# Kernel tuning notes

Measured on AMD Instinct MI355X. Metric: run time of the kernel, lower is better.

The kernel has to match this reference:

```python
import jax, jax.numpy as jnp
import numpy as np

N_NODES = 100000
N_EDGES = 1600000
NEG_SLOPE = 0.01  # F.leaky_relu default


def _param(key, shape, scale=0.05):
    return jax.random.normal(key, shape, dtype=jnp.float32) * scale


def setup_inputs() -> dict:
    key = jax.random.key(0)
    ks = jax.random.split(key, 32)
    inp = {
        "x": jax.random.normal(ks[0], (N_NODES, 64), dtype=jnp.float32),
        "edge_index": jax.random.randint(ks[1], (2, N_EDGES), 0, N_NODES, dtype=jnp.int64),
        # encoder SAGEConv params: lin_l (neighbors, with bias) + lin_r (root)
        "ggn1_Wl": _param(ks[2], (128, 64)), "ggn1_b": jnp.zeros((128,), jnp.float32), "ggn1_Wr": _param(ks[3], (128, 64)),
        "ggn2_Wl": _param(ks[4], (128, 128)), "ggn2_b": jnp.zeros((128,), jnp.float32), "ggn2_Wr": _param(ks[5], (128, 128)),
        "ggn3_Wl": _param(ks[6], (128, 128)), "ggn3_b": jnp.zeros((128,), jnp.float32), "ggn3_Wr": _param(ks[7], (128, 128)),
        "tr2_W": _param(ks[8], (64, 128)), "tr2_b": jnp.zeros((64,), jnp.float32),
        # decoder
        "dec1_W": _param(ks[9], (128, 64)), "dec1_b": jnp.zeros((128,), jnp.float32),
        "dec2_Wl": _param(ks[10], (128, 128)), "dec2_b": jnp.zeros((128,), jnp.float32), "dec2_Wr": _param(ks[11], (128, 128)),
        "dec3_Wl": _param(ks[12], (64, 128)), "dec3_b": jnp.zeros((64,), jnp.float32), "dec3_Wr": _param(ks[13], (64, 128)),
        "dec4_Wl": _param(ks[14], (3, 64)), "dec4_b": jnp.zeros((3,), jnp.float32), "dec4_Wr": _param(ks[15], (3, 64)),
    }
    return inp


def _sage(x, src, dst, Wl, b, Wr, n):
    # PyG SAGEConv (aggr='mean'): lin_l(mean_{j->i} x_j) + lin_r(x_i)
    msgs = x[src]                                              # [E, d] gather
    s = jax.ops.segment_sum(msgs, dst, num_segments=n)          # [N, d]
    cnt = jax.ops.segment_sum(jnp.ones((src.shape[0], 1), x.dtype), dst, num_segments=n)
    mean = s / jnp.maximum(cnt, 1.0)
    return mean @ Wl.T + b + x @ Wr.T


def _leaky(h):
    return jnp.where(h > 0, h, NEG_SLOPE * h)


def reference(x, edge_index,
              ggn1_Wl, ggn1_b, ggn1_Wr,
              ggn2_Wl, ggn2_b, ggn2_Wr,
              ggn3_Wl, ggn3_b, ggn3_Wr,
              tr2_W, tr2_b,
              dec1_W, dec1_b,
              dec2_Wl, dec2_b, dec2_Wr,
              dec3_Wl, dec3_b, dec3_Wr,
              dec4_Wl, dec4_b, dec4_Wr):
    n = x.shape[0]
    src, dst = edge_index[0], edge_index[1]  # source_to_target flow
    # --- encode (dropout = identity, deterministic reference) ---
    h = jnp.tanh(_sage(x, src, dst, ggn1_Wl, ggn1_b, ggn1_Wr, n))
    h = jnp.tanh(_sage(h, src, dst, ggn2_Wl, ggn2_b, ggn2_Wr, n))
    h = jnp.tanh(_sage(h, src, dst, ggn3_Wl, ggn3_b, ggn3_Wr, n))
    mu = h @ tr2_W.T + tr2_b
    logvar = mu  # module applies the same tr2 twice
    z = mu       # reparametrize in eval mode returns mu
    # --- decode ---
    o = _leaky(z @ dec1_W.T + dec1_b)
    o = _leaky(_sage(o, src, dst, dec2_Wl, dec2_b, dec2_Wr, n))
    o = jnp.tanh(_sage(o, src, dst, dec3_Wl, dec3_b, dec3_Wr, n))
    z2 = _sage(o, src, dst, dec4_Wl, dec4_b, dec4_Wr, n)
    return (z2[:, :2], z2[:, 2], mu, logvar)
```

## Files before the change

kernel.cpp:

```cpp
#include <hip/hip_runtime.h>
#include <cmath>


constexpr int ACT_NONE = 0, ACT_TANH = 1, ACT_LEAKY = 2;
constexpr int SCAN_CHUNK = 4096;

typedef __attribute__((ext_vector_type(8))) __bf16 bf16x8;
typedef __attribute__((ext_vector_type(4))) float f32x4;

__device__ __forceinline__ unsigned short f2h(float x) {
  _Float16 h = (_Float16)x;
  unsigned short u;
  __builtin_memcpy(&u, &h, 2);
  return u;
}
__device__ __forceinline__ float hlo(unsigned int u) {
  unsigned short s = (unsigned short)(u & 0xffffu);
  _Float16 h;
  __builtin_memcpy(&h, &s, 2);
  return (float)h;
}
__device__ __forceinline__ float hhi(unsigned int u) {
  unsigned short s = (unsigned short)(u >> 16);
  _Float16 h;
  __builtin_memcpy(&h, &s, 2);
  return (float)h;
}

__global__ __launch_bounds__(256) void count_rank_kernel(const int* __restrict__ dst,
                                                         int* __restrict__ cnt,
                                                         int* __restrict__ rank, int E) {
  int e = blockIdx.x * 256 + threadIdx.x;
  if (e < E) rank[e] = atomicAdd(&cnt[dst[e]], 1);
}

__global__ __launch_bounds__(1024) void scan_blk_kernel(const int* __restrict__ cnt,
                                                        int* __restrict__ rowptr,
                                                        float* __restrict__ inv,
                                                        int* __restrict__ bsum, int n) {
  __shared__ int wsum[17];
  const int lane = threadIdx.x & 63;
  const int wid = threadIdx.x >> 6;
  const int i0 = blockIdx.x * SCAN_CHUNK + threadIdx.x * 4;
  int v[4];
  if (i0 + 3 < n) {
    int4 t = *(const int4*)(cnt + i0);
    v[0] = t.x; v[1] = t.y; v[2] = t.z; v[3] = t.w;
  } else {
#pragma unroll
    for (int j = 0; j < 4; ++j) v[j] = (i0 + j < n) ? cnt[i0 + j] : 0;
  }
#pragma unroll
  for (int j = 0; j < 4; ++j)
    if (i0 + j < n) inv[i0 + j] = 1.0f / (float)(v[j] > 1 ? v[j] : 1);
  const int s = v[0] + v[1] + v[2] + v[3];
  int x = s;
#pragma unroll
  for (int off = 1; off < 64; off <<= 1) {
    int t = __shfl_up(x, off);
    if (lane >= off) x += t;
  }
  if (lane == 63) wsum[wid + 1] = x;
  __syncthreads();
  if (threadIdx.x == 0) {
    wsum[0] = 0;
    for (int w = 1; w <= 16; ++w) wsum[w] += wsum[w - 1];
    bsum[blockIdx.x] = wsum[16];
  }
  __syncthreads();
  int p = wsum[wid] + x - s;
#pragma unroll
  for (int j = 0; j < 4; ++j) {
    if (i0 + j < n) rowptr[i0 + j] = p;
    p += v[j];
  }
}

__global__ __launch_bounds__(1024) void scan_sums_kernel(int* __restrict__ bsum,
                                                         int* __restrict__ rowptr,
                                                         int nb, int n) {
  __shared__ int wsum[17];
  const int lane = threadIdx.x & 63;
  const int wid = threadIdx.x >> 6;
  const int v = (threadIdx.x < nb) ? bsum[threadIdx.x] : 0;
  int x = v;
#pragma unroll
  for (int off = 1; off < 64; off <<= 1) {
    int t = __shfl_up(x, off);
    if (lane >= off) x += t;
  }
  if (lane == 63) wsum[wid + 1] = x;
  __syncthreads();
  if (threadIdx.x == 0) {
    wsum[0] = 0;
    for (int w = 1; w <= 16; ++w) wsum[w] += wsum[w - 1];
    rowptr[n] = wsum[16];
  }
  __syncthreads();
  if (threadIdx.x < nb) bsum[threadIdx.x] = wsum[wid] + x - v;
}

__global__ __launch_bounds__(1024) void scan_add_kernel(int* __restrict__ rowptr,
                                                        const int* __restrict__ bsum,
                                                        int n) {
  const int off = bsum[blockIdx.x];
  const int i0 = blockIdx.x * SCAN_CHUNK + threadIdx.x * 4;
  if (i0 + 3 < n) {
    int4 t = *(const int4*)(rowptr + i0);
    t.x += off; t.y += off; t.z += off; t.w += off;
    *(int4*)(rowptr + i0) = t;
  } else {
    for (int j = 0; j < 4; ++j)
      if (i0 + j < n) rowptr[i0 + j] += off;
  }
}

__global__ __launch_bounds__(256) void scatter_kernel(const int* __restrict__ src,
                                                      const int* __restrict__ dst,
                                                      const int* __restrict__ rowptr,
                                                      const int* __restrict__ rank,
                                                      int* __restrict__ esrc, int E) {
  int e = blockIdx.x * 256 + threadIdx.x;
  if (e < E) esrc[rowptr[dst[e]] + rank[e]] = src[e];
}

template <int D>
__global__ __launch_bounds__(256) void gather_mean_kernel(
    const float* __restrict__ in, const int* __restrict__ esrc,
    const int* __restrict__ rowptr, const float* __restrict__ inv,
    float* __restrict__ meanb, int n) {
  const int node = blockIdx.x * 4 + (threadIdx.x >> 6);
  const int lane = threadIdx.x & 63;
  if (node >= n) return;
  const int beg = rowptr[node];
  const int end = rowptr[node + 1];
  const float iv = inv[node];
  if constexpr (D == 128) {
    const float2* base = (const float2*)in;
    float a0x = 0.f, a0y = 0.f, a1x = 0.f, a1y = 0.f;
    float a2x = 0.f, a2y = 0.f, a3x = 0.f, a3y = 0.f;
    for (int b = beg; b < end; b += 64) {
      int m = end - b;
      if (m > 64) m = 64;
      int myi = (lane < m) ? esrc[b + lane] : 0;
      int s = 0;
      for (; s + 4 <= m; s += 4) {
        int i0 = __shfl(myi, s);
        int i1 = __shfl(myi, s + 1);
        int i2 = __shfl(myi, s + 2);
        int i3 = __shfl(myi, s + 3);
        float2 v0 = base[(size_t)i0 * 64 + lane];
        float2 v1 = base[(size_t)i1 * 64 + lane];
        float2 v2 = base[(size_t)i2 * 64 + lane];
        float2 v3 = base[(size_t)i3 * 64 + lane];
        a0x += v0.x; a0y += v0.y;
        a1x += v1.x; a1y += v1.y;
        a2x += v2.x; a2y += v2.y;
        a3x += v3.x; a3y += v3.y;
      }
      for (; s < m; ++s) {
        int i0 = __shfl(myi, s);
        float2 v0 = base[(size_t)i0 * 64 + lane];
        a0x += v0.x; a0y += v0.y;
      }
    }
    float2 r;
    r.x = ((a0x + a1x) + (a2x + a3x)) * iv;
    r.y = ((a0y + a1y) + (a2y + a3y)) * iv;
    ((float2*)meanb)[(size_t)node * 64 + lane] = r;
  } else {
    float a0 = 0.f, a1 = 0.f, a2 = 0.f, a3 = 0.f;
    for (int b = beg; b < end; b += 64) {
      int m = end - b;
      if (m > 64) m = 64;
      int myi = (lane < m) ? esrc[b + lane] : 0;
      int s = 0;
      for (; s + 4 <= m; s += 4) {
        int i0 = __shfl(myi, s);
        int i1 = __shfl(myi, s + 1);
        int i2 = __shfl(myi, s + 2);
        int i3 = __shfl(myi, s + 3);
        a0 += in[(size_t)i0 * 64 + lane];
        a1 += in[(size_t)i1 * 64 + lane];
        a2 += in[(size_t)i2 * 64 + lane];
        a3 += in[(size_t)i3 * 64 + lane];
      }
      for (; s < m; ++s) {
        int i0 = __shfl(myi, s);
        a0 += in[(size_t)i0 * 64 + lane];
      }
    }
    meanb[(size_t)node * 64 + lane] = ((a0 + a1) + (a2 + a3)) * iv;
  }
}

__global__ __launch_bounds__(256) void gather_s16_kernel(
    const unsigned short* __restrict__ inq, const int* __restrict__ esrc,
    const int* __restrict__ rowptr, const float* __restrict__ inv,
    float* __restrict__ meanb, int n) {
  const int node = blockIdx.x * 4 + (threadIdx.x >> 6);
  const int lane = threadIdx.x & 63;
  if (node >= n) return;
  const int beg = rowptr[node];
  const int end = rowptr[node + 1];
  const float iv = inv[node] * (1.0f / 32767.0f);
  const unsigned int* bu = (const unsigned int*)inq;
  int a0l = 0, a0h = 0, a1l = 0, a1h = 0;
  int a2l = 0, a2h = 0, a3l = 0, a3h = 0;
  for (int b = beg; b < end; b += 64) {
    int m = end - b;
    if (m > 64) m = 64;
    int myi = (lane < m) ? esrc[b + lane] : 0;
    int s = 0;
    for (; s + 4 <= m; s += 4) {
      int i0 = __shfl(myi, s);
      int i1 = __shfl(myi, s + 1);
      int i2 = __shfl(myi, s + 2);
      int i3 = __shfl(myi, s + 3);
      unsigned int u0 = bu[(size_t)i0 * 64 + lane];
      unsigned int u1 = bu[(size_t)i1 * 64 + lane];
      unsigned int u2 = bu[(size_t)i2 * 64 + lane];
      unsigned int u3 = bu[(size_t)i3 * 64 + lane];
      a0l += (int)(short)u0; a0h += ((int)u0) >> 16;
      a1l += (int)(short)u1; a1h += ((int)u1) >> 16;
      a2l += (int)(short)u2; a2h += ((int)u2) >> 16;
      a3l += (int)(short)u3; a3h += ((int)u3) >> 16;
    }
    for (; s < m; ++s) {
      int i0 = __shfl(myi, s);
      unsigned int u0 = bu[(size_t)i0 * 64 + lane];
      a0l += (int)(short)u0; a0h += ((int)u0) >> 16;
    }
  }
  float2 r;
  r.x = (float)((a0l + a1l) + (a2l + a3l)) * iv;
  r.y = (float)((a0h + a1h) + (a2h + a3h)) * iv;
  ((float2*)meanb)[(size_t)node * 64 + lane] = r;
}

template <int D>
__global__ __launch_bounds__(256) void gather_h_kernel(
    const unsigned short* __restrict__ inh, const int* __restrict__ esrc,
    const int* __restrict__ rowptr, const float* __restrict__ inv,
    float* __restrict__ meanb, int n) {
  const int node = blockIdx.x * 4 + (threadIdx.x >> 6);
  const int lane = threadIdx.x & 63;
  if (node >= n) return;
  const int beg = rowptr[node];
  const int end = rowptr[node + 1];
  const float iv = inv[node];
  const unsigned int* bu = (const unsigned int*)inh;
  if constexpr (D == 128) {
    float a0x = 0.f, a0y = 0.f, a1x = 0.f, a1y = 0.f;
    float a2x = 0.f, a2y = 0.f, a3x = 0.f, a3y = 0.f;
    for (int b = beg; b < end; b += 64) {
      int m = end - b;
      if (m > 64) m = 64;
      int myi = (lane < m) ? esrc[b + lane] : 0;
      int s = 0;
      for (; s + 4 <= m; s += 4) {
        int i0 = __shfl(myi, s);
        int i1 = __shfl(myi, s + 1);
        int i2 = __shfl(myi, s + 2);
        int i3 = __shfl(myi, s + 3);
        unsigned int u0 = bu[(size_t)i0 * 64 + lane];
        unsigned int u1 = bu[(size_t)i1 * 64 + lane];
        unsigned int u2 = bu[(size_t)i2 * 64 + lane];
        unsigned int u3 = bu[(size_t)i3 * 64 + lane];
        a0x += hlo(u0); a0y += hhi(u0);
        a1x += hlo(u1); a1y += hhi(u1);
        a2x += hlo(u2); a2y += hhi(u2);
        a3x += hlo(u3); a3y += hhi(u3);
      }
      for (; s < m; ++s) {
        int i0 = __shfl(myi, s);
        unsigned int u0 = bu[(size_t)i0 * 64 + lane];
        a0x += hlo(u0); a0y += hhi(u0);
      }
    }
    float2 r;
    r.x = ((a0x + a1x) + (a2x + a3x)) * iv;
    r.y = ((a0y + a1y) + (a2y + a3y)) * iv;
    ((float2*)meanb)[(size_t)node * 64 + lane] = r;
  } else {
    const int half = lane >> 5;
    const int hl = lane & 31;
    float ax = 0.f, ay = 0.f, bx = 0.f, by = 0.f;
    for (int b = beg; b < end; b += 64) {
      int m = end - b;
      if (m > 64) m = 64;
      int myi = (lane < m) ? esrc[b + lane] : 0;
      int s = 0;
      for (; s + 4 <= m; s += 4) {
        int i0 = __shfl(myi, s + half);
        int i1 = __shfl(myi, s + 2 + half);
        unsigned int u0 = bu[(size_t)i0 * 32 + hl];
        unsigned int u1 = bu[(size_t)i1 * 32 + hl];
        ax += hlo(u0); ay += hhi(u0);
        bx += hlo(u1); by += hhi(u1);
      }
      for (; s < m; s += 2) {
        int t = s + half;
        if (t < m) {
          int i0 = __shfl(myi, t);
          unsigned int u0 = bu[(size_t)i0 * 32 + hl];
          ax += hlo(u0); ay += hhi(u0);
        }
      }
    }
    float sx = ax + bx, sy = ay + by;
    sx += __shfl_xor(sx, 32);
    sy += __shfl_xor(sy, 32);
    if (half == 0)
      ((float2*)meanb)[(size_t)node * 32 + hl] = make_float2(sx * iv, sy * iv);
  }
}

__global__ __launch_bounds__(256) void gather_mean4_kernel(
    const float* __restrict__ y4, const int* __restrict__ esrc,
    const int* __restrict__ rowptr, const float* __restrict__ inv,
    float* __restrict__ mean4, int n) {
  int i = blockIdx.x * 256 + threadIdx.x;
  if (i >= n) return;
  const int beg = rowptr[i], end = rowptr[i + 1];
  const float iv = inv[i];
  float sx = 0.f, sy = 0.f, sz = 0.f;
  const float4* b = (const float4*)y4;
  for (int j = beg; j < end; ++j) {
    float4 v = b[esrc[j]];
    sx += v.x; sy += v.y; sz += v.z;
  }
  ((float4*)mean4)[i] = make_float4(sx * iv, sy * iv, sz * iv, 0.f);
}

__device__ __forceinline__ void split_bf16(float x, __bf16& h, __bf16& l) {
  h = (__bf16)x;
  l = (__bf16)(x - (float)h);
}

template <int DI, int DO, int ACT, bool AGG, bool ADDMEAN, bool BIAS, int SH>
__global__ __launch_bounds__(256) void node_mfma_kernel(
    const float* __restrict__ in, const float* __restrict__ meanb,
    const float* __restrict__ Wl, const float* __restrict__ Wr,
    const float* __restrict__ bias, float* __restrict__ out,
    float* __restrict__ out2, unsigned short* __restrict__ outh, int n) {
  constexpr int BM = 128;
  constexpr int KC = 32;
  constexpr int KS = 40;
  constexpr int CT = DO / 16;
  __shared__ __align__(16) __bf16 As_hi[BM * KS];
  __shared__ __align__(16) __bf16 As_lo[BM * KS];
  __shared__ __align__(16) __bf16 Ws_hi[DO * KS];
  __shared__ __align__(16) __bf16 Ws_lo[DO * KS];

  const int wv = threadIdx.x >> 6;
  const int lane = threadIdx.x & 63;
  const int lm = lane & 15;
  const int lq = lane >> 4;
  const int row0 = blockIdx.x * BM;

  f32x4 acc[2][CT];
#pragma unroll
  for (int rt = 0; rt < 2; ++rt)
#pragma unroll
    for (int ct = 0; ct < CT; ++ct) acc[rt][ct] = (f32x4){0.f, 0.f, 0.f, 0.f};

  const int nphase = AGG ? 2 : 1;
  for (int phase = 0; phase < nphase; ++phase) {
    const float* W = (phase == 0) ? Wr : Wl;
    const float* Amat = (phase == 0) ? in : meanb;
    for (int k0 = 0; k0 < DI; k0 += KC) {
      {
        const int r = threadIdx.x >> 1;
        const int kb = (threadIdx.x & 1) * 16;
        const int row = row0 + r;
        float v[16];
        if (row < n) {
          const float4* p = (const float4*)(Amat + (size_t)row * DI + k0 + kb);
#pragma unroll
          for (int i = 0; i < 4; ++i) {
            float4 t = p[i];
            v[4 * i + 0] = t.x; v[4 * i + 1] = t.y;
            v[4 * i + 2] = t.z; v[4 * i + 3] = t.w;
          }
        } else {
#pragma unroll
          for (int i = 0; i < 16; ++i) v[i] = 0.f;
        }
        bf16x8 hi[2], lo[2];
#pragma unroll
        for (int g = 0; g < 2; ++g)
#pragma unroll
          for (int i = 0; i < 8; ++i) {
            __bf16 h, l;
            split_bf16(v[g * 8 + i], h, l);
            hi[g][i] = h; lo[g][i] = l;
          }
        *(bf16x8*)(&As_hi[r * KS + kb]) = hi[0];
        *(bf16x8*)(&As_hi[r * KS + kb + 8]) = hi[1];
        *(bf16x8*)(&As_lo[r * KS + kb]) = lo[0];
        *(bf16x8*)(&As_lo[r * KS + kb + 8]) = lo[1];
      }
      if constexpr (DO == 128) {
        const int c = threadIdx.x >> 1;
        const int kb = (threadIdx.x & 1) * 16;
        const float4* p = (const float4*)(W + (size_t)c * DI + k0 + kb);
        float v[16];
#pragma unroll
        for (int i = 0; i < 4; ++i) {
          float4 t = p[i];
          v[4 * i + 0] = t.x; v[4 * i + 1] = t.y;
          v[4 * i + 2] = t.z; v[4 * i + 3] = t.w;
        }
        bf16x8 hi[2], lo[2];
#pragma unroll
        for (int g = 0; g < 2; ++g)
#pragma unroll
          for (int i = 0; i < 8; ++i) {
            __bf16 h, l;
            split_bf16(v[g * 8 + i], h, l);
            hi[g][i] = h; lo[g][i] = l;
          }
        *(bf16x8*)(&Ws_hi[c * KS + kb]) = hi[0];
        *(bf16x8*)(&Ws_hi[c * KS + kb + 8]) = hi[1];
        *(bf16x8*)(&Ws_lo[c * KS + kb]) = lo[0];
        *(bf16x8*)(&Ws_lo[c * KS + kb + 8]) = lo[1];
      } else {
        const int c = threadIdx.x >> 2;
        const int kb = (threadIdx.x & 3) * 8;
        const float4* p = (const float4*)(W + (size_t)c * DI + k0 + kb);
        float v[8];
#pragma unroll
        for (int i = 0; i < 2; ++i) {
          float4 t = p[i];
          v[4 * i + 0] = t.x; v[4 * i + 1] = t.y;
          v[4 * i + 2] = t.z; v[4 * i + 3] = t.w;
        }
        bf16x8 hi, lo;
#pragma unroll
        for (int i = 0; i < 8; ++i) {
          __bf16 h, l;
          split_bf16(v[i], h, l);
          hi[i] = h; lo[i] = l;
        }
        *(bf16x8*)(&Ws_hi[c * KS + kb]) = hi;
        *(bf16x8*)(&Ws_lo[c * KS + kb]) = lo;
      }
      __syncthreads();
      const int kb = lq * 8;
      bf16x8 ah[2], al[2];
#pragma unroll
      for (int rt = 0; rt < 2; ++rt) {
        const int r = wv * 32 + rt * 16 + lm;
        ah[rt] = *(const bf16x8*)(&As_hi[r * KS + kb]);
        al[rt] = *(const bf16x8*)(&As_lo[r * KS + kb]);
      }
#pragma unroll
      for (int ct = 0; ct < CT; ++ct) {
        const int c = ct * 16 + lm;
        bf16x8 bh = *(const bf16x8*)(&Ws_hi[c * KS + kb]);
        bf16x8 bl = *(const bf16x8*)(&Ws_lo[c * KS + kb]);
#pragma unroll
        for (int rt = 0; rt < 2; ++rt) {
          acc[rt][ct] = __builtin_amdgcn_mfma_f32_16x16x32_bf16(ah[rt], bh, acc[rt][ct], 0, 0, 0);
          acc[rt][ct] = __builtin_amdgcn_mfma_f32_16x16x32_bf16(al[rt], bh, acc[rt][ct], 0, 0, 0);
          acc[rt][ct] = __builtin_amdgcn_mfma_f32_16x16x32_bf16(ah[rt], bl, acc[rt][ct], 0, 0, 0);
        }
      }
      __syncthreads();
    }
  }

#pragma unroll
  for (int rt = 0; rt < 2; ++rt)
#pragma unroll
    for (int ct = 0; ct < CT; ++ct) {
      const int col = ct * 16 + lm;
      const float bval = BIAS ? bias[col] : 0.f;
      f32x4 a = acc[rt][ct];
#pragma unroll
      for (int r = 0; r < 4; ++r) {
        const int row = row0 + wv * 32 + rt * 16 + lq * 4 + r;
        if (row < n) {
          float t = a[r] + bval;
          if (ADDMEAN) t += meanb[(size_t)row * DO + col];
          if (ACT == ACT_TANH) t = tanhf(t);
          else if (ACT == ACT_LEAKY) t = (t > 0.f) ? t : 0.01f * t;
          if (out) out[(size_t)row * DO + col] = t;
          if (out2) out2[(size_t)row * DO + col] = t;
          if constexpr (SH == 1) {
            if (outh) outh[(size_t)row * DO + col] = f2h(t);
          } else if constexpr (SH == 2) {
            if (outh)
              outh[(size_t)row * DO + col] =
                  (unsigned short)(short)__builtin_rintf(t * 32767.0f);
          }
        }
      }
    }
}

__global__ __launch_bounds__(256) void dec4_pre_kernel(
    const float* __restrict__ hB, const float* __restrict__ Wl,
    float* __restrict__ y4, int n) {
  const int node = blockIdx.x * 4 + (threadIdx.x >> 6);
  const int lane = threadIdx.x & 63;
  if (node >= n) return;
  float v = hB[(size_t)node * 64 + lane];
  float p0 = v * Wl[lane];
  float p1 = v * Wl[64 + lane];
  float p2 = v * Wl[128 + lane];
#pragma unroll
  for (int off = 32; off >= 1; off >>= 1) {
    p0 += __shfl_xor(p0, off);
    p1 += __shfl_xor(p1, off);
    p2 += __shfl_xor(p2, off);
  }
  if (lane == 0) ((float4*)y4)[node] = make_float4(p0, p1, p2, 0.f);
}

__global__ __launch_bounds__(256) void dec4_final_kernel(
    const float* __restrict__ hB, const float* __restrict__ mean4,
    const float* __restrict__ Wr, const float* __restrict__ bias,
    float* __restrict__ out, int n) {
  const int node = blockIdx.x * 4 + (threadIdx.x >> 6);
  const int lane = threadIdx.x & 63;
  if (node >= n) return;
  float v = hB[(size_t)node * 64 + lane];
  float p0 = v * Wr[lane];
  float p1 = v * Wr[64 + lane];
  float p2 = v * Wr[128 + lane];
#pragma unroll
  for (int off = 32; off >= 1; off >>= 1) {
    p0 += __shfl_xor(p0, off);
    p1 += __shfl_xor(p1, off);
    p2 += __shfl_xor(p2, off);
  }
  if (lane == 0) {
    float4 m = ((const float4*)mean4)[node];
    out[2 * (size_t)node]     = p0 + m.x + bias[0];
    out[2 * (size_t)node + 1] = p1 + m.y + bias[1];
    out[2 * (size_t)n + node] = p2 + m.z + bias[2];
  }
}

extern "C" void kernel_launch(void* const* d_in, const int* in_sizes, int n_in,
                              void* d_out, int out_size, void* d_ws, size_t ws_size,
                              hipStream_t stream) {
  const float* x = (const float*)d_in[0];
  const int* ei = (const int*)d_in[1];
  const int N = in_sizes[0] / 64;
  const int E = in_sizes[1] / 2;
  const int* src = ei;
  const int* dst = ei + E;
  const float* g1Wl = (const float*)d_in[2];
  const float* g1b  = (const float*)d_in[3];
  const float* g1Wr = (const float*)d_in[4];
  const float* g2Wl = (const float*)d_in[5];
  const float* g2b  = (const float*)d_in[6];
  const float* g2Wr = (const float*)d_in[7];
  const float* g3Wl = (const float*)d_in[8];
  const float* g3b  = (const float*)d_in[9];
  const float* g3Wr = (const float*)d_in[10];
  const float* t2W  = (const float*)d_in[11];
  const float* t2b  = (const float*)d_in[12];
  const float* d1W  = (const float*)d_in[13];
  const float* d1b  = (const float*)d_in[14];
  const float* d2Wl = (const float*)d_in[15];
  const float* d2b  = (const float*)d_in[16];
  const float* d2Wr = (const float*)d_in[17];
  const float* d3Wl = (const float*)d_in[18];
  const float* d3b  = (const float*)d_in[19];
  const float* d3Wr = (const float*)d_in[20];
  const float* d4Wl = (const float*)d_in[21];
  const float* d4b  = (const float*)d_in[22];
  const float* d4Wr = (const float*)d_in[23];

  float* ws = (float*)d_ws;
  const size_t N128 = (size_t)N * 128;
  float* hA   = ws;
  float* hB   = ws + N128;
  float* mean = ws + 2 * N128;
  int*   cnt  = (int*)(ws + 3 * N128);
  float* inv  = ws + 3 * N128 + N;
  int*   rowp = (int*)(ws + 3 * N128 + 2 * (size_t)N);
  int*   rank = (int*)(ws + 3 * N128 + 3 * (size_t)N + 1);
  int*   esrc = rank + E;
  unsigned short* shB = (unsigned short*)(esrc + E);
  unsigned short* shC = shB + N128;

  float* y4    = mean;
  float* mean4 = mean + (size_t)N * 4;
  int*   bsum  = (int*)mean;

  float* out = (float*)d_out;
  float* mu  = out + 3 * (size_t)N;
  float* lv  = mu + 64 * (size_t)N;

  const int NB = (N + 127) / 128;
  const int GB = (N + 3) / 4;
  const int SB = (N + SCAN_CHUNK - 1) / SCAN_CHUNK;

  hipMemsetAsync(cnt, 0, (size_t)N * sizeof(int), stream);
  count_rank_kernel<<<(E + 255) / 256, 256, 0, stream>>>(dst, cnt, rank, E);
  scan_blk_kernel<<<SB, 1024, 0, stream>>>(cnt, rowp, inv, bsum, N);
  scan_sums_kernel<<<1, 1024, 0, stream>>>(bsum, rowp, SB, N);
  scan_add_kernel<<<SB, 1024, 0, stream>>>(rowp, bsum, N);
  scatter_kernel<<<(E + 255) / 256, 256, 0, stream>>>(src, dst, rowp, rank, esrc, E);

  gather_mean_kernel<64><<<GB, 256, 0, stream>>>(x, esrc, rowp, inv, mean, N);
  node_mfma_kernel<64, 128, ACT_TANH, true, false, true, 2><<<NB, 256, 0, stream>>>(
      x, mean, g1Wl, g1Wr, g1b, hA, nullptr, shB, N);

  gather_s16_kernel<<<GB, 256, 0, stream>>>(shB, esrc, rowp, inv, mean, N);
  node_mfma_kernel<128, 128, ACT_TANH, true, false, true, 2><<<NB, 256, 0, stream>>>(
      hA, mean, g2Wl, g2Wr, g2b, hB, nullptr, shB, N);

  gather_s16_kernel<<<GB, 256, 0, stream>>>(shB, esrc, rowp, inv, mean, N);
  node_mfma_kernel<128, 128, ACT_TANH, true, false, true, 0><<<NB, 256, 0, stream>>>(
      hB, mean, g3Wl, g3Wr, g3b, hA, nullptr, nullptr, N);

  node_mfma_kernel<128, 64, ACT_NONE, false, false, true, 0><<<NB, 256, 0, stream>>>(
      hA, nullptr, nullptr, t2W, t2b, mu, lv, nullptr, N);

  node_mfma_kernel<64, 128, ACT_LEAKY, false, false, true, 1><<<NB, 256, 0, stream>>>(
      mu, nullptr, nullptr, d1W, d1b, hB, nullptr, shB, N);

  gather_h_kernel<128><<<GB, 256, 0, stream>>>(shB, esrc, rowp, inv, mean, N);
  node_mfma_kernel<128, 128, ACT_LEAKY, true, false, true, 0><<<NB, 256, 0, stream>>>(
      hB, mean, d2Wl, d2Wr, d2b, hA, nullptr, nullptr, N);

  node_mfma_kernel<128, 64, ACT_NONE, false, false, false, 1><<<NB, 256, 0, stream>>>(
      hA, nullptr, nullptr, d3Wl, nullptr, nullptr, nullptr, shC, N);
  gather_h_kernel<64><<<GB, 256, 0, stream>>>(shC, esrc, rowp, inv, mean, N);
  node_mfma_kernel<128, 64, ACT_TANH, false, true, true, 0><<<NB, 256, 0, stream>>>(
      hA, mean, nullptr, d3Wr, d3b, hB, nullptr, nullptr, N);

  dec4_pre_kernel<<<GB, 256, 0, stream>>>(hB, d4Wl, y4, N);
  gather_mean4_kernel<<<(N + 255) / 256, 256, 0, stream>>>(y4, esrc, rowp, inv, mean4, N);
  dec4_final_kernel<<<GB, 256, 0, stream>>>(hB, mean4, d4Wr, d4b, out, N);
}
```

Measured before the change: 1.018 ms.

## Store activations and weights as pre-split bf16 hi/lo pairs for MFMA GEMMs

Node GEMM kernels now read activations, means and weights already split into bf16 high/low halves. The producers do the split: separate kernels for x and the weights, and the epilogues of the gather and GEMM kernels for everything else. This removes the per-tile fp32 load plus split work inside every GEMM block, and halves nothing in bytes, since hi+lo equals the size of fp32. It adds two extra launches and splitting work in the producers, and the workspace layout and aliasing are rearranged.

```diff
diff --git a/kernel.cpp b/kernel.cpp
--- a/kernel.cpp
+++ b/kernel.cpp
@@ -7,6 +7,7 @@
 
 typedef __attribute__((ext_vector_type(8))) __bf16 bf16x8;
 typedef __attribute__((ext_vector_type(4))) float f32x4;
+typedef __attribute__((ext_vector_type(4))) unsigned short u16x4;
 
 __device__ __forceinline__ unsigned short f2h(float x) {
   _Float16 h = (_Float16)x;
@@ -25,6 +26,69 @@
   _Float16 h;
   __builtin_memcpy(&h, &s, 2);
   return (float)h;
+}
+__device__ __forceinline__ void split_bf16(float x, __bf16& h, __bf16& l) {
+  h = (__bf16)x;
+  l = (__bf16)(x - (float)h);
+}
+__device__ __forceinline__ unsigned short b2u(__bf16 b) {
+  unsigned short u;
+  __builtin_memcpy(&u, &b, 2);
+  return u;
+}
+
+__global__ __launch_bounds__(256) void split_x_kernel(const float* __restrict__ in,
+                                                      __bf16* __restrict__ hi,
+                                                      __bf16* __restrict__ lo, int total) {
+  int i = (blockIdx.x * 256 + threadIdx.x) * 4;
+  if (i >= total) return;
+  float4 v = *(const float4*)(in + i);
+  float vv[4] = {v.x, v.y, v.z, v.w};
+  u16x4 h, l;
+#pragma unroll
+  for (int j = 0; j < 4; ++j) {
+    __bf16 hb, lb;
+    split_bf16(vv[j], hb, lb);
+    h[j] = b2u(hb);
+    l[j] = b2u(lb);
+  }
+  *(u16x4*)(hi + i) = h;
+  *(u16x4*)(lo + i) = l;
+}
+
+__global__ __launch_bounds__(256) void split_w_kernel(
+    const float* p0, const float* p1, const float* p2, const float* p3,
+    const float* p4, const float* p5, const float* p6, const float* p7,
+    const float* p8, const float* p9, const float* p10, const float* p11,
+    __bf16* __restrict__ hi, __bf16* __restrict__ lo) {
+  int b = blockIdx.x;
+  const float* src;
+  int boff, doff;
+  if      (b < 8)   { src = p0;  boff = b;       doff = 0; }
+  else if (b < 16)  { src = p1;  boff = b - 8;   doff = 8192; }
+  else if (b < 32)  { src = p2;  boff = b - 16;  doff = 16384; }
+  else if (b < 48)  { src = p3;  boff = b - 32;  doff = 32768; }
+  else if (b < 64)  { src = p4;  boff = b - 48;  doff = 49152; }
+  else if (b < 80)  { src = p5;  boff = b - 64;  doff = 65536; }
+  else if (b < 88)  { src = p6;  boff = b - 80;  doff = 81920; }
+  else if (b < 96)  { src = p7;  boff = b - 88;  doff = 90112; }
+  else if (b < 112) { src = p8;  boff = b - 96;  doff = 98304; }
+  else if (b < 128) { src = p9;  boff = b - 112; doff = 114688; }
+  else if (b < 136) { src = p10; boff = b - 128; doff = 131072; }
+  else              { src = p11; boff = b - 136; doff = 139264; }
+  int i = boff * 1024 + threadIdx.x * 4;
+  float4 v = *(const float4*)(src + i);
+  float vv[4] = {v.x, v.y, v.z, v.w};
+  u16x4 h, l;
+#pragma unroll
+  for (int j = 0; j < 4; ++j) {
+    __bf16 hb, lb;
+    split_bf16(vv[j], hb, lb);
+    h[j] = b2u(hb);
+    l[j] = b2u(lb);
+  }
+  *(u16x4*)(hi + doff + i) = h;
+  *(u16x4*)(lo + doff + i) = l;
 }
 
 __global__ __launch_bounds__(256) void count_rank_kernel(const int* __restrict__ dst,
@@ -124,80 +188,48 @@
   if (e < E) esrc[rowptr[dst[e]] + rank[e]] = src[e];
 }
 
-template <int D>
-__global__ __launch_bounds__(256) void gather_mean_kernel(
+__global__ __launch_bounds__(256) void gather_f32s_kernel(
     const float* __restrict__ in, const int* __restrict__ esrc,
     const int* __restrict__ rowptr, const float* __restrict__ inv,
-    float* __restrict__ meanb, int n) {
+    __bf16* __restrict__ Mhi, __bf16* __restrict__ Mlo, int n) {
   const int node = blockIdx.x * 4 + (threadIdx.x >> 6);
   const int lane = threadIdx.x & 63;
   if (node >= n) return;
   const int beg = rowptr[node];
   const int end = rowptr[node + 1];
   const float iv = inv[node];
-  if constexpr (D == 128) {
-    const float2* base = (const float2*)in;
-    float a0x = 0.f, a0y = 0.f, a1x = 0.f, a1y = 0.f;
-    float a2x = 0.f, a2y = 0.f, a3x = 0.f, a3y = 0.f;
-    for (int b = beg; b < end; b += 64) {
-      int m = end - b;
-      if (m > 64) m = 64;
-      int myi = (lane < m) ? esrc[b + lane] : 0;
-      int s = 0;
-      for (; s + 4 <= m; s += 4) {
-        int i0 = __shfl(myi, s);
-        int i1 = __shfl(myi, s + 1);
-        int i2 = __shfl(myi, s + 2);
-        int i3 = __shfl(myi, s + 3);
-        float2 v0 = base[(size_t)i0 * 64 + lane];
-        float2 v1 = base[(size_t)i1 * 64 + lane];
-        float2 v2 = base[(size_t)i2 * 64 + lane];
-        float2 v3 = base[(size_t)i3 * 64 + lane];
-        a0x += v0.x; a0y += v0.y;
-        a1x += v1.x; a1y += v1.y;
-        a2x += v2.x; a2y += v2.y;
-        a3x += v3.x; a3y += v3.y;
-      }
-      for (; s < m; ++s) {
-        int i0 = __shfl(myi, s);
-        float2 v0 = base[(size_t)i0 * 64 + lane];
-        a0x += v0.x; a0y += v0.y;
-      }
-    }
-    float2 r;
-    r.x = ((a0x + a1x) + (a2x + a3x)) * iv;
-    r.y = ((a0y + a1y) + (a2y + a3y)) * iv;
-    ((float2*)meanb)[(size_t)node * 64 + lane] = r;
-  } else {
-    float a0 = 0.f, a1 = 0.f, a2 = 0.f, a3 = 0.f;
-    for (int b = beg; b < end; b += 64) {
-      int m = end - b;
-      if (m > 64) m = 64;
-      int myi = (lane < m) ? esrc[b + lane] : 0;
-      int s = 0;
-      for (; s + 4 <= m; s += 4) {
-        int i0 = __shfl(myi, s);
-        int i1 = __shfl(myi, s + 1);
-        int i2 = __shfl(myi, s + 2);
-        int i3 = __shfl(myi, s + 3);
-        a0 += in[(size_t)i0 * 64 + lane];
-        a1 += in[(size_t)i1 * 64 + lane];
-        a2 += in[(size_t)i2 * 64 + lane];
-        a3 += in[(size_t)i3 * 64 + lane];
-      }
-      for (; s < m; ++s) {
-        int i0 = __shfl(myi, s);
-        a0 += in[(size_t)i0 * 64 + lane];
-      }
-    }
-    meanb[(size_t)node * 64 + lane] = ((a0 + a1) + (a2 + a3)) * iv;
-  }
+  float a0 = 0.f, a1 = 0.f, a2 = 0.f, a3 = 0.f;
+  for (int b = beg; b < end; b += 64) {
+    int m = end - b;
+    if (m > 64) m = 64;
+    int myi = (lane < m) ? esrc[b + lane] : 0;
+    int s = 0;
+    for (; s + 4 <= m; s += 4) {
+      int i0 = __shfl(myi, s);
+      int i1 = __shfl(myi, s + 1);
+      int i2 = __shfl(myi, s + 2);
+      int i3 = __shfl(myi, s + 3);
+      a0 += in[(size_t)i0 * 64 + lane];
+      a1 += in[(size_t)i1 * 64 + lane];
+      a2 += in[(size_t)i2 * 64 + lane];
+      a3 += in[(size_t)i3 * 64 + lane];
+    }
+    for (; s < m; ++s) {
+      int i0 = __shfl(myi, s);
+      a0 += in[(size_t)i0 * 64 + lane];
+    }
+  }
+  float mv = ((a0 + a1) + (a2 + a3)) * iv;
+  __bf16 h, l;
+  split_bf16(mv, h, l);
+  Mhi[(size_t)node * 64 + lane] = h;
+  Mlo[(size_t)node * 64 + lane] = l;
 }
 
 __global__ __launch_bounds__(256) void gather_s16_kernel(
     const unsigned short* __restrict__ inq, const int* __restrict__ esrc,
     const int* __restrict__ rowptr, const float* __restrict__ inv,
-    float* __restrict__ meanb, int n) {
+    __bf16* __restrict__ Mhi, __bf16* __restrict__ Mlo, int n) {
   const int node = blockIdx.x * 4 + (threadIdx.x >> 6);
   const int lane = threadIdx.x & 63;
   if (node >= n) return;
@@ -232,17 +264,21 @@
       a0l += (int)(short)u0; a0h += ((int)u0) >> 16;
     }
   }
-  float2 r;
-  r.x = (float)((a0l + a1l) + (a2l + a3l)) * iv;
-  r.y = (float)((a0h + a1h) + (a2h + a3h)) * iv;
-  ((float2*)meanb)[(size_t)node * 64 + lane] = r;
-}
-
-template <int D>
-__global__ __launch_bounds__(256) void gather_h_kernel(
+  float rx = (float)((a0l + a1l) + (a2l + a3l)) * iv;
+  float ry = (float)((a0h + a1h) + (a2h + a3h)) * iv;
+  __bf16 h0, l0, h1, l1;
+  split_bf16(rx, h0, l0);
+  split_bf16(ry, h1, l1);
+  ((unsigned int*)Mhi)[(size_t)node * 64 + lane] =
+      (unsigned int)b2u(h0) | ((unsigned int)b2u(h1) << 16);
+  ((unsigned int*)Mlo)[(size_t)node * 64 + lane] =
+      (unsigned int)b2u(l0) | ((unsigned int)b2u(l1) << 16);
+}
+
+__global__ __launch_bounds__(256) void gather_h128_kernel(
     const unsigned short* __restrict__ inh, const int* __restrict__ esrc,
     const int* __restrict__ rowptr, const float* __restrict__ inv,
-    float* __restrict__ meanb, int n) {
+    __bf16* __restrict__ Mhi, __bf16* __restrict__ Mlo, int n) {
   const int node = blockIdx.x * 4 + (threadIdx.x >> 6);
   const int lane = threadIdx.x & 63;
   if (node >= n) return;
@@ -250,70 +286,85 @@
   const int end = rowptr[node + 1];
   const float iv = inv[node];
   const unsigned int* bu = (const unsigned int*)inh;
-  if constexpr (D == 128) {
-    float a0x = 0.f, a0y = 0.f, a1x = 0.f, a1y = 0.f;
-    float a2x = 0.f, a2y = 0.f, a3x = 0.f, a3y = 0.f;
-    for (int b = beg; b < end; b += 64) {
-      int m = end - b;
-      if (m > 64) m = 64;
-      int myi = (lane < m) ? esrc[b + lane] : 0;
-      int s = 0;
-      for (; s + 4 <= m; s += 4) {
-        int i0 = __shfl(myi, s);
-        int i1 = __shfl(myi, s + 1);
-        int i2 = __shfl(myi, s + 2);
-        int i3 = __shfl(myi, s + 3);
-        unsigned int u0 = bu[(size_t)i0 * 64 + lane];
-        unsigned int u1 = bu[(size_t)i1 * 64 + lane];
-        unsigned int u2 = bu[(size_t)i2 * 64 + lane];
-        unsigned int u3 = bu[(size_t)i3 * 64 + lane];
-        a0x += hlo(u0); a0y += hhi(u0);
-        a1x += hlo(u1); a1y += hhi(u1);
-        a2x += hlo(u2); a2y += hhi(u2);
-        a3x += hlo(u3); a3y += hhi(u3);
+  float a0x = 0.f, a0y = 0.f, a1x = 0.f, a1y = 0.f;
+  float a2x = 0.f, a2y = 0.f, a3x = 0.f, a3y = 0.f;
+  for (int b = beg; b < end; b += 64) {
+    int m = end - b;
+    if (m > 64) m = 64;
+    int myi = (lane < m) ? esrc[b + lane] : 0;
+    int s = 0;
+    for (; s + 4 <= m; s += 4) {
+      int i0 = __shfl(myi, s);
+      int i1 = __shfl(myi, s + 1);
+      int i2 = __shfl(myi, s + 2);
+      int i3 = __shfl(myi, s + 3);
+      unsigned int u0 = bu[(size_t)i0 * 64 + lane];
+      unsigned int u1 = bu[(size_t)i1 * 64 + lane];
+      unsigned int u2 = bu[(size_t)i2 * 64 + lane];
+      unsigned int u3 = bu[(size_t)i3 * 64 + lane];
+      a0x += hlo(u0); a0y += hhi(u0);
+      a1x += hlo(u1); a1y += hhi(u1);
+      a2x += hlo(u2); a2y += hhi(u2);
+      a3x += hlo(u3); a3y += hhi(u3);
+    }
+    for (; s < m; ++s) {
+      int i0 = __shfl(myi, s);
+      unsigned int u0 = bu[(size_t)i0 * 64 + lane];
+      a0x += hlo(u0); a0y += hhi(u0);
+    }
+  }
+  float rx = ((a0x + a1x) + (a2x + a3x)) * iv;
+  float ry = ((a0y + a1y) + (a2y + a3y)) * iv;
+  __bf16 h0, l0, h1, l1;
+  split_bf16(rx, h0, l0);
+  split_bf16(ry, h1, l1);
+  ((unsigned int*)Mhi)[(size_t)node * 64 + lane] =
+      (unsigned int)b2u(h0) | ((unsigned int)b2u(h1) << 16);
+  ((unsigned int*)Mlo)[(size_t)node * 64 + lane] =
+      (unsigned int)b2u(l0) | ((unsigned int)b2u(l1) << 16);
+}
+
+__global__ __launch_bounds__(256) void gather_h64_kernel(
+    const unsigned short* __restrict__ inh, const int* __restrict__ esrc,
+    const int* __restrict__ rowptr, const float* __restrict__ inv,
+    float* __restrict__ meanb, int n) {
+  const int node = blockIdx.x * 4 + (threadIdx.x >> 6);
+  const int lane = threadIdx.x & 63;
+  if (node >= n) return;
+  const int beg = rowptr[node];
+  const int end = rowptr[node + 1];
+  const float iv = inv[node];
+  const unsigned int* bu = (const unsigned int*)inh;
+  const int half = lane >> 5;
+  const int hl = lane & 31;
+  float ax = 0.f, ay = 0.f, bx = 0.f, by = 0.f;
+  for (int b = beg; b < end; b += 64) {
+    int m = end - b;
+    if (m > 64) m = 64;
+    int myi = (lane < m) ? esrc[b + lane] : 0;
+    int s = 0;
+    for (; s + 4 <= m; s += 4) {
+      int i0 = __shfl(myi, s + half);
+      int i1 = __shfl(myi, s + 2 + half);
+      unsigned int u0 = bu[(size_t)i0 * 32 + hl];
+      unsigned int u1 = bu[(size_t)i1 * 32 + hl];
+      ax += hlo(u0); ay += hhi(u0);
+      bx += hlo(u1); by += hhi(u1);
+    }
+    for (; s < m; s += 2) {
+      int t = s + half;
+      if (t < m) {
+        int i0 = __shfl(myi, t);
+        unsigned int u0 = bu[(size_t)i0 * 32 + hl];
+        ax += hlo(u0); ay += hhi(u0);
       }
-      for (; s < m; ++s) {
-        int i0 = __shfl(myi, s);
-        unsigned int u0 = bu[(size_t)i0 * 64 + lane];
-        a0x += hlo(u0); a0y += hhi(u0);
-      }
-    }
-    float2 r;
-    r.x = ((a0x + a1x) + (a2x + a3x)) * iv;
-    r.y = ((a0y + a1y) + (a2y + a3y)) * iv;
-    ((float2*)meanb)[(size_t)node * 64 + lane] = r;
-  } else {
-    const int half = lane >> 5;
-    const int hl = lane & 31;
-    float ax = 0.f, ay = 0.f, bx = 0.f, by = 0.f;
-    for (int b = beg; b < end; b += 64) {
-      int m = end - b;
-      if (m > 64) m = 64;
-      int myi = (lane < m) ? esrc[b + lane] : 0;
-      int s = 0;
-      for (; s + 4 <= m; s += 4) {
-        int i0 = __shfl(myi, s + half);
-        int i1 = __shfl(myi, s + 2 + half);
-        unsigned int u0 = bu[(size_t)i0 * 32 + hl];
-        unsigned int u1 = bu[(size_t)i1 * 32 + hl];
-        ax += hlo(u0); ay += hhi(u0);
-        bx += hlo(u1); by += hhi(u1);
-      }
-      for (; s < m; s += 2) {
-        int t = s + half;
-        if (t < m) {
-          int i0 = __shfl(myi, t);
-          unsigned int u0 = bu[(size_t)i0 * 32 + hl];
-          ax += hlo(u0); ay += hhi(u0);
-        }
-      }
-    }
-    float sx = ax + bx, sy = ay + by;
-    sx += __shfl_xor(sx, 32);
-    sy += __shfl_xor(sy, 32);
-    if (half == 0)
-      ((float2*)meanb)[(size_t)node * 32 + hl] = make_float2(sx * iv, sy * iv);
-  }
+    }
+  }
+  float sx = ax + bx, sy = ay + by;
+  sx += __shfl_xor(sx, 32);
+  sy += __shfl_xor(sy, 32);
+  if (half == 0)
+    ((float2*)meanb)[(size_t)node * 32 + hl] = make_float2(sx * iv, sy * iv);
 }
 
 __global__ __launch_bounds__(256) void gather_mean4_kernel(
@@ -333,17 +384,16 @@
   ((float4*)mean4)[i] = make_float4(sx * iv, sy * iv, sz * iv, 0.f);
 }
 
-__device__ __forceinline__ void split_bf16(float x, __bf16& h, __bf16& l) {
-  h = (__bf16)x;
-  l = (__bf16)(x - (float)h);
-}
-
-template <int DI, int DO, int ACT, bool AGG, bool ADDMEAN, bool BIAS, int SH>
+template <int DI, int DO, int ACT, bool AGG, bool ADDMEAN, bool BIAS, int SH, bool OSPLIT>
 __global__ __launch_bounds__(256) void node_mfma_kernel(
-    const float* __restrict__ in, const float* __restrict__ meanb,
-    const float* __restrict__ Wl, const float* __restrict__ Wr,
-    const float* __restrict__ bias, float* __restrict__ out,
-    float* __restrict__ out2, unsigned short* __restrict__ outh, int n) {
+    const __bf16* __restrict__ Ahi, const __bf16* __restrict__ Alo,
+    const __bf16* __restrict__ Mhi, const __bf16* __restrict__ Mlo,
+    const __bf16* __restrict__ Wrhi, const __bf16* __restrict__ Wrlo,
+    const __bf16* __restrict__ Wlhi, const __bf16* __restrict__ Wllo,
+    const float* __restrict__ bias, const float* __restrict__ meanF,
+    float* __restrict__ out, float* __restrict__ out2,
+    unsigned short* __restrict__ outh,
+    __bf16* __restrict__ ohi, __bf16* __restrict__ olo, int n) {
   constexpr int BM = 128;
   constexpr int KC = 32;
   constexpr int KS = 40;
@@ -367,84 +417,48 @@
 
   const int nphase = AGG ? 2 : 1;
   for (int phase = 0; phase < nphase; ++phase) {
-    const float* W = (phase == 0) ? Wr : Wl;
-    const float* Amat = (phase == 0) ? in : meanb;
+    const __bf16* AH = (phase == 0) ? Ahi : Mhi;
+    const __bf16* AL = (phase == 0) ? Alo : Mlo;
+    const __bf16* WH = (phase == 0) ? Wrhi : Wlhi;
+    const __bf16* WL = (phase == 0) ? Wrlo : Wllo;
     for (int k0 = 0; k0 < DI; k0 += KC) {
       {
         const int r = threadIdx.x >> 1;
         const int kb = (threadIdx.x & 1) * 16;
         const int row = row0 + r;
-        float v[16];
+        bf16x8 h0, h1, l0, l1;
         if (row < n) {
-          const float4* p = (const float4*)(Amat + (size_t)row * DI + k0 + kb);
-#pragma unroll
-          for (int i = 0; i < 4; ++i) {
-            float4 t = p[i];
-            v[4 * i + 0] = t.x; v[4 * i + 1] = t.y;
-            v[4 * i + 2] = t.z; v[4 * i + 3] = t.w;
-          }
+          const bf16x8* ph = (const bf16x8*)(AH + (size_t)row * DI + k0 + kb);
+          const bf16x8* pl = (const bf16x8*)(AL + (size_t)row * DI + k0 + kb);
+          h0 = ph[0]; h1 = ph[1];
+          l0 = pl[0]; l1 = pl[1];
         } else {
-#pragma unroll
-          for (int i = 0; i < 16; ++i) v[i] = 0.f;
+          bf16x8 z;
+#pragma unroll
+          for (int j = 0; j < 8; ++j) z[j] = (__bf16)0.f;
+          h0 = h1 = l0 = l1 = z;
         }
-        bf16x8 hi[2], lo[2];
-#pragma unroll
-        for (int g = 0; g < 2; ++g)
-#pragma unroll
-          for (int i = 0; i < 8; ++i) {
-            __bf16 h, l;
-            split_bf16(v[g * 8 + i], h, l);
-            hi[g][i] = h; lo[g][i] = l;
-          }
-        *(bf16x8*)(&As_hi[r * KS + kb]) = hi[0];
-        *(bf16x8*)(&As_hi[r * KS + kb + 8]) = hi[1];
-        *(bf16x8*)(&As_lo[r * KS + kb]) = lo[0];
-        *(bf16x8*)(&As_lo[r * KS + kb + 8]) = lo[1];
+        *(bf16x8*)(&As_hi[r * KS + kb]) = h0;
+        *(bf16x8*)(&As_hi[r * KS + kb + 8]) = h1;
+        *(bf16x8*)(&As_lo[r * KS + kb]) = l0;
+        *(bf16x8*)(&As_lo[r * KS + kb + 8]) = l1;
       }
       if constexpr (DO == 128) {
         const int c = threadIdx.x >> 1;
         const int kb = (threadIdx.x & 1) * 16;
-        const float4* p = (const float4*)(W + (size_t)c * DI + k0 + kb);
-        float v[16];
-#pragma unroll
-        for (int i = 0; i < 4; ++i) {
-          float4 t = p[i];
-          v[4 * i + 0] = t.x; v[4 * i + 1] = t.y;
-          v[4 * i + 2] = t.z; v[4 * i + 3] = t.w;
-        }
-        bf16x8 hi[2], lo[2];
-#pragma unroll
-        for (int g = 0; g < 2; ++g)
-#pragma unroll
-          for (int i = 0; i < 8; ++i) {
-            __bf16 h, l;
-            split_bf16(v[g * 8 + i], h, l);
-            hi[g][i] = h; lo[g][i] = l;
-          }
-        *(bf16x8*)(&Ws_hi[c * KS + kb]) = hi[0];
-        *(bf16x8*)(&Ws_hi[c * KS + kb + 8]) = hi[1];
-        *(bf16x8*)(&Ws_lo[c * KS + kb]) = lo[0];
-        *(bf16x8*)(&Ws_lo[c * KS + kb + 8]) = lo[1];
+        const bf16x8* ph = (const bf16x8*)(WH + (size_t)c * DI + k0 + kb);
+        const bf16x8* pl = (const bf16x8*)(WL + (size_t)c * DI + k0 + kb);
+        *(bf16x8*)(&Ws_hi[c * KS + kb]) = ph[0];
+        *(bf16x8*)(&Ws_hi[c * KS + kb + 8]) = ph[1];
+        *(bf16x8*)(&Ws_lo[c * KS + kb]) = pl[0];
+        *(bf16x8*)(&Ws_lo[c * KS + kb + 8]) = pl[1];
       } else {
         const int c = threadIdx.x >> 2;
         const int kb = (threadIdx.x & 3) * 8;
-        const float4* p = (const float4*)(W + (size_t)c * DI + k0 + kb);
-        float v[8];
-#pragma unroll
-        for (int i = 0; i < 2; ++i) {
-          float4 t = p[i];
-          v[4 * i + 0] = t.x; v[4 * i + 1] = t.y;
-          v[4 * i + 2] = t.z; v[4 * i + 3] = t.w;
-        }
-        bf16x8 hi, lo;
-#pragma unroll
-        for (int i = 0; i < 8; ++i) {
-          __bf16 h, l;
-          split_bf16(v[i], h, l);
-          hi[i] = h; lo[i] = l;
-        }
-        *(bf16x8*)(&Ws_hi[c * KS + kb]) = hi;
-        *(bf16x8*)(&Ws_lo[c * KS + kb]) = lo;
+        *(bf16x8*)(&Ws_hi[c * KS + kb]) =
+            *(const bf16x8*)(WH + (size_t)c * DI + k0 + kb);
+        *(bf16x8*)(&Ws_lo[c * KS + kb]) =
+            *(const bf16x8*)(WL + (size_t)c * DI + k0 + kb);
       }
       __syncthreads();
       const int kb = lq * 8;
@@ -483,7 +497,7 @@
         const int row = row0 + wv * 32 + rt * 16 + lq * 4 + r;
         if (row < n) {
           float t = a[r] + bval;
-          if (ADDMEAN) t += meanb[(size_t)row * DO + col];
+          if (ADDMEAN) t += meanF[(size_t)row * DO + col];
           if (ACT == ACT_TANH) t = tanhf(t);
           else if (ACT == ACT_LEAKY) t = (t > 0.f) ? t : 0.01f * t;
           if (out) out[(size_t)row * DO + col] = t;
@@ -494,6 +508,12 @@
             if (outh)
               outh[(size_t)row * DO + col] =
                   (unsigned short)(short)__builtin_rintf(t * 32767.0f);
+          }
+          if constexpr (OSPLIT) {
+            __bf16 hb, lb;
+            split_bf16(t, hb, lb);
+            ohi[(size_t)row * DO + col] = hb;
+            olo[(size_t)row * DO + col] = lb;
           }
         }
       }
@@ -576,22 +596,40 @@
   const float* d4b  = (const float*)d_in[22];
   const float* d4Wr = (const float*)d_in[23];
 
-  float* ws = (float*)d_ws;
+  const size_t N64 = (size_t)N * 64;
   const size_t N128 = (size_t)N * 128;
-  float* hA   = ws;
-  float* hB   = ws + N128;
-  float* mean = ws + 2 * N128;
-  int*   cnt  = (int*)(ws + 3 * N128);
-  float* inv  = ws + 3 * N128 + N;
-  int*   rowp = (int*)(ws + 3 * N128 + 2 * (size_t)N);
-  int*   rank = (int*)(ws + 3 * N128 + 3 * (size_t)N + 1);
-  int*   esrc = rank + E;
-  unsigned short* shB = (unsigned short*)(esrc + E);
-  unsigned short* shC = shB + N128;
-
-  float* y4    = mean;
-  float* mean4 = mean + (size_t)N * 4;
-  int*   bsum  = (int*)mean;
+
+  char* w = (char*)d_ws;
+  auto alloc = [&](size_t bytes) {
+    char* p = w;
+    w += (bytes + 255) & ~(size_t)255;
+    return p;
+  };
+  __bf16* Ahi = (__bf16*)alloc(N128 * 2);
+  __bf16* Alo = (__bf16*)alloc(N128 * 2);
+  __bf16* Bhi = (__bf16*)alloc(N128 * 2);
+  __bf16* Blo = (__bf16*)alloc(N128 * 2);
+  float*  meanF = (float*)alloc(N128 * 4);
+  __bf16* xhi = (__bf16*)alloc(N64 * 2);
+  __bf16* xlo = (__bf16*)alloc(N64 * 2);
+  __bf16* Whi = (__bf16*)alloc(147456 * 2);
+  __bf16* Wlo = (__bf16*)alloc(147456 * 2);
+  int*    cnt = (int*)alloc((size_t)N * 4);
+  float*  inv = (float*)alloc((size_t)N * 4);
+  int*    rowp = (int*)alloc(((size_t)N + 1) * 4);
+  int*    rank = (int*)alloc((size_t)E * 4);
+  int*    esrc = (int*)alloc((size_t)E * 4);
+  unsigned short* shB = (unsigned short*)alloc(N128 * 2);
+
+  __bf16* Mhi = (__bf16*)meanF;
+  __bf16* Mlo = Mhi + N128;
+  int*    bsum = (int*)meanF;
+  float*  y4 = meanF;
+  float*  mean4 = meanF + 4 * (size_t)N;
+  float*  hBf = meanF + N64;
+  __bf16* muhi = xhi;
+  __bf16* mulo = xlo;
+  unsigned short* shC = (unsigned short*)xhi;
 
   float* out = (float*)d_out;
   float* mu  = out + 3 * (size_t)N;
@@ -600,6 +638,23 @@
   const int NB = (N + 127) / 128;
   const int GB = (N + 3) / 4;
   const int SB = (N + SCAN_CHUNK - 1) / SCAN_CHUNK;
+
+  const __bf16 *W_g1Wl_h = Whi + 0,      *W_g1Wl_l = Wlo + 0;
+  const __bf16 *W_g1Wr_h = Whi + 8192,   *W_g1Wr_l = Wlo + 8192;
+  const __bf16 *W_g2Wl_h = Whi + 16384,  *W_g2Wl_l = Wlo + 16384;
+  const __bf16 *W_g2Wr_h = Whi + 32768,  *W_g2Wr_l = Wlo + 32768;
+  const __bf16 *W_g3Wl_h = Whi + 49152,  *W_g3Wl_l = Wlo + 49152;
+  const __bf16 *W_g3Wr_h = Whi + 65536,  *W_g3Wr_l = Wlo + 65536;
+  const __bf16 *W_t2W_h  = Whi + 81920,  *W_t2W_l  = Wlo + 81920;
+  const __bf16 *W_d1W_h  = Whi + 90112,  *W_d1W_l  = Wlo + 90112;
+  const __bf16 *W_d2Wl_h = Whi + 98304,  *W_d2Wl_l = Wlo + 98304;
+  const __bf16 *W_d2Wr_h = Whi + 114688, *W_d2Wr_l = Wlo + 114688;
+  const __bf16 *W_d3Wl_h = Whi + 131072, *W_d3Wl_l = Wlo + 131072;
+  const __bf16 *W_d3Wr_h = Whi + 139264, *W_d3Wr_l = Wlo + 139264;
+
+  split_x_kernel<<<(int)((N64 + 1023) / 1024), 256, 0, stream>>>(x, xhi, xlo, (int)N64);
+  split_w_kernel<<<144, 256, 0, stream>>>(g1Wl, g1Wr, g2Wl, g2Wr, g3Wl, g3Wr,
+                                          t2W, d1W, d2Wl, d2Wr, d3Wl, d3Wr, Whi, Wlo);
 
   hipMemsetAsync(cnt, 0, (size_t)N * sizeof(int), stream);
   count_rank_kernel<<<(E + 255) / 256, 256, 0, stream>>>(dst, cnt, rank, E);
@@ -608,35 +663,43 @@
   scan_add_kernel<<<SB, 1024, 0, stream>>>(rowp, bsum, N);
   scatter_kernel<<<(E + 255) / 256, 256, 0, stream>>>(src, dst, rowp, rank, esrc, E);
 
-  gather_mean_kernel<64><<<GB, 256, 0, stream>>>(x, esrc, rowp, inv, mean, N);
-  node_mfma_kernel<64, 128, ACT_TANH, true, false, true, 2><<<NB, 256, 0, stream>>>(
-      x, mean, g1Wl, g1Wr, g1b, hA, nullptr, shB, N);
-
-  gather_s16_kernel<<<GB, 256, 0, stream>>>(shB, esrc, rowp, inv, mean, N);
-  node_mfma_kernel<128, 128, ACT_TANH, true, false, true, 2><<<NB, 256, 0, stream>>>(
-      hA, mean, g2Wl, g2Wr, g2b, hB, nullptr, shB, N);
-
-  gather_s16_kernel<<<GB, 256, 0, stream>>>(shB, esrc, rowp, inv, mean, N);
-  node_mfma_kernel<128, 128, ACT_TANH, true, false, true, 0><<<NB, 256, 0, stream>>>(
-      hB, mean, g3Wl, g3Wr, g3b, hA, nullptr, nullptr, N);
-
-  node_mfma_kernel<128, 64, ACT_NONE, false, false, true, 0><<<NB, 256, 0, stream>>>(
-      hA, nullptr, nullptr, t2W, t2b, mu, lv, nullptr, N);
-
-  node_mfma_kernel<64, 128, ACT_LEAKY, false, false, true, 1><<<NB, 256, 0, stream>>>(
-      mu, nullptr, nullptr, d1W, d1b, hB, nullptr, shB, N);
-
-  gather_h_kernel<128><<<GB, 256, 0, stream>>>(shB, esrc, rowp, inv, mean, N);
-  node_mfma_kernel<128, 128, ACT_LEAKY, true, false, true, 0><<<NB, 256, 0, stream>>>(
-      hB, mean, d2Wl, d2Wr, d2b, hA, nullptr, nullptr, N);
-
-  node_mfma_kernel<128, 64, ACT_NONE, false, false, false, 1><<<NB, 256, 0, stream>>>(
-      hA, nullptr, nullptr, d3Wl, nullptr, nullptr, nullptr, shC, N);
-  gather_h_kernel<64><<<GB, 256, 0, stream>>>(shC, esrc, rowp, inv, mean, N);
-  node_mfma_kernel<128, 64, ACT_TANH, false, true, true, 0><<<NB, 256, 0, stream>>>(
-      hA, mean, nullptr, d3Wr, d3b, hB, nullptr, nullptr, N);
-
-  dec4_pre_kernel<<<GB, 256, 0, stream>>>(hB, d4Wl, y4, N);
+  gather_f32s_kernel<<<GB, 256, 0, stream>>>(x, esrc, rowp, inv, Mhi, Mlo, N);
+  node_mfma_kernel<64, 128, ACT_TANH, true, false, true, 2, true><<<NB, 256, 0, stream>>>(
+      xhi, xlo, Mhi, Mlo, W_g1Wr_h, W_g1Wr_l, W_g1Wl_h, W_g1Wl_l, g1b, nullptr,
+      nullptr, nullptr, shB, Ahi, Alo, N);
+
+  gather_s16_kernel<<<GB, 256, 0, stream>>>(shB, esrc, rowp, inv, Mhi, Mlo, N);
+  node_mfma_kernel<128, 128, ACT_TANH, true, false, true, 2, true><<<NB, 256, 0, stream>>>(
+      Ahi, Alo, Mhi, Mlo, W_g2Wr_h, W_g2Wr_l, W_g2Wl_h, W_g2Wl_l, g2b, nullptr,
+      nullptr, nullptr, shB, Bhi, Blo, N);
+
+  gather_s16_kernel<<<GB, 256, 0, stream>>>(shB, esrc, rowp, inv, Mhi, Mlo, N);
+  node_mfma_kernel<128, 128, ACT_TANH, true, false, true, 0, true><<<NB, 256, 0, stream>>>(
+      Bhi, Blo, Mhi, Mlo, W_g3Wr_h, W_g3Wr_l, W_g3Wl_h, W_g3Wl_l, g3b, nullptr,
+      nullptr, nullptr, nullptr, Ahi, Alo, N);
+
+  node_mfma_kernel<128, 64, ACT_NONE, false, false, true, 0, true><<<NB, 256, 0, stream>>>(
+      Ahi, Alo, nullptr, nullptr, W_t2W_h, W_t2W_l, nullptr, nullptr, t2b, nullptr,
+      mu, lv, nullptr, muhi, mulo, N);
+
+  node_mfma_kernel<64, 128, ACT_LEAKY, false, false, true, 1, true><<<NB, 256, 0, stream>>>(
+      muhi, mulo, nullptr, nullptr, W_d1W_h, W_d1W_l, nullptr, nullptr, d1b, nullptr,
+      nullptr, nullptr, shB, Bhi, Blo, N);
+
+  gather_h128_kernel<<<GB, 256, 0, stream>>>(shB, esrc, rowp, inv, Mhi, Mlo, N);
+  node_mfma_kernel<128, 128, ACT_LEAKY, true, false, true, 0, true><<<NB, 256, 0, stream>>>(
+      Bhi, Blo, Mhi, Mlo, W_d2Wr_h, W_d2Wr_l, W_d2Wl_h, W_d2Wl_l, d2b, nullptr,
+      nullptr, nullptr, nullptr, Ahi, Alo, N);
+
+  node_mfma_kernel<128, 64, ACT_NONE, false, false, false, 1, false><<<NB, 256, 0, stream>>>(
+      Ahi, Alo, nullptr, nullptr, W_d3Wl_h, W_d3Wl_l, nullptr, nullptr, nullptr, nullptr,
+      nullptr, nullptr, shC, nullptr, nullptr, N);
+  gather_h64_kernel<<<GB, 256, 0, stream>>>(shC, esrc, rowp, inv, meanF, N);
+  node_mfma_kernel<128, 64, ACT_TANH, false, true, true, 0, false><<<NB, 256, 0, stream>>>(
+      Ahi, Alo, nullptr, nullptr, W_d3Wr_h, W_d3Wr_l, nullptr, nullptr, d3b, meanF,
+      hBf, nullptr, nullptr, nullptr, nullptr, N);
+
+  dec4_pre_kernel<<<GB, 256, 0, stream>>>(hBf, d4Wl, y4, N);
   gather_mean4_kernel<<<(N + 255) / 256, 256, 0, stream>>>(y4, esrc, rowp, inv, mean4, N);
-  dec4_final_kernel<<<GB, 256, 0, stream>>>(hB, mean4, d4Wr, d4b, out, N);
-}
+  dec4_final_kernel<<<GB, 256, 0, stream>>>(hBf, mean4, d4Wr, d4b, out, N);
+}
```

After: 998.1 us. Within noise of the previous version (-1.9%).
